# Performance work log

Hardware: AMD Instinct MI355X
Metric: run time of the kernel (lower is better)

The kernel has to match this reference:

```python
import jax, jax.numpy as jnp
import numpy as np

B, C, H, W = 16, 1024, 64, 64
CH = C // 2
LN_EPS = 1e-5  # F.layer_norm default eps

def setup_inputs() -> dict:
    key = jax.random.key(0)
    ks = jax.random.split(key, 5)
    x = jax.random.normal(ks[0], (B, C, H, W), dtype=jnp.float32)
    # 1x1 conv weights, shape (out_ch, in_ch)
    w_qr = jax.random.normal(ks[1], (1, C), dtype=jnp.float32) * 0.02
    w_vr = jax.random.normal(ks[2], (CH, C), dtype=jnp.float32) * 0.02
    w_ql = jax.random.normal(ks[3], (CH, C), dtype=jnp.float32) * 0.02
    w_vl = jax.random.normal(ks[4], (CH, C), dtype=jnp.float32) * 0.02
    return {"x": x, "w_qr": w_qr, "w_vr": w_vr, "w_ql": w_ql, "w_vl": w_vl}

def reference(x, w_qr, w_vr, w_ql, w_vl):
    b, c, h, w = x.shape
    ch, hw = c // 2, h * w
    # mmcv ConvModule: 1x1 conv (no bias, no norm) + default ReLU activation
    conv = lambda wt: jax.nn.relu(jnp.einsum('bchw,oc->bohw', x, wt))

    # --- spatial attention branch ---
    input_x = conv(w_vr).reshape(b, ch, hw)                       # (b, ch, hw)
    mask = jax.nn.softmax(conv(w_qr).reshape(b, hw), axis=1)      # (b, hw)
    context = jnp.einsum('bcn,bn->bc', input_x, mask)             # (b, ch)
    # layer_norm over (ch,1,1) -> normalize over channel dim, no affine
    mu = jnp.mean(context, axis=1, keepdims=True)
    var = jnp.mean((context - mu) ** 2, axis=1, keepdims=True)
    spatial_attn = jax.nn.sigmoid((context - mu) * jax.lax.rsqrt(var + LN_EPS))[:, :, None]  # (b, ch, 1)

    # --- channel attention branch ---
    g_x = conv(w_ql)                                              # (b, ch, h, w)
    avg_x = jax.nn.softmax(jnp.mean(g_x, axis=(2, 3)), axis=1)    # (b, ch)
    theta_x = conv(w_vl).reshape(b, ch, hw)                       # (b, ch, hw)
    channel_attn = jax.nn.sigmoid(jnp.einsum('bc,bcn->bn', avg_x, theta_x))[:, None, :]  # (b, 1, hw)

    # --- combine ---
    sequence = (spatial_attn * channel_attn).reshape(b, ch, h, w)  # outer product (b, ch, hw)
    parallel = (channel_attn + spatial_attn).reshape(b, ch, h, w)  # broadcast sum
    sk_attn = jnp.concatenate([sequence, parallel], axis=1)        # (b, c, h, w)
    return x * sk_attn + x
```

## Files before the change

### kernel.cpp

```cpp
#include <hip/hip_runtime.h>
#include <cstdint>
#include <cstddef>

#define BATCH 16
#define CIN   1024
#define CH    512
#define HW    4096

static constexpr float LN_EPS = 1e-5f;

typedef __bf16 bf16x8 __attribute__((ext_vector_type(8)));
typedef float  f32x4  __attribute__((ext_vector_type(4)));

__device__ __forceinline__ float sigmoidf_(float v) { return 1.0f / (1.0f + __expf(-v)); }

__device__ __forceinline__ unsigned short f2bf(float f) {
    union { float f; uint32_t u; } c; c.f = f;
    uint32_t r = (c.u + 0x7fffu + ((c.u >> 16) & 1u)) >> 16;
    return (unsigned short)r;
}

#define GLOAD_LDS16(g, l)                                                  \
    __builtin_amdgcn_global_load_lds(                                      \
        (const __attribute__((address_space(1))) void*)(g),                \
        (__attribute__((address_space(3))) void*)(l), 16, 0, 0)

__global__ __launch_bounds__(256) void transpose_convert(
    const float* __restrict__ x, const float* __restrict__ wqr,
    unsigned short* __restrict__ xt, float* __restrict__ maskpre)
{
    const int b  = blockIdx.z;
    const int c0 = blockIdx.y * 64;
    const int n0 = blockIdx.x * 64;
    __shared__ float t[64][65];
    const int tid = threadIdx.x;
    const int tx = tid & 15, ty = tid >> 4;
    const float* xb = x + ((size_t)b * CIN + c0) * HW + n0;
#pragma unroll
    for (int rr = 0; rr < 4; ++rr) {
        const int row = ty + rr * 16;
        float4 v = *(const float4*)(xb + (size_t)row * HW + tx * 4);
        t[row][tx * 4 + 0] = v.x; t[row][tx * 4 + 1] = v.y;
        t[row][tx * 4 + 2] = v.z; t[row][tx * 4 + 3] = v.w;
    }
    __syncthreads();
    const int n  = tid >> 2;
    const int cp = (tid & 3) * 16;
    __align__(16) unsigned short tmp[16];
    float part = 0.f;
#pragma unroll
    for (int i = 0; i < 16; ++i) {
        const float v = t[cp + i][n];
        tmp[i] = f2bf(v);
        part = fmaf(wqr[c0 + cp + i], v, part);
    }
    unsigned short* dst = xt + ((size_t)b * HW + n0 + n) * CIN + c0 + cp;
    ((uint4*)dst)[0] = ((const uint4*)tmp)[0];
    ((uint4*)dst)[1] = ((const uint4*)tmp)[1];
    part += __shfl_xor(part, 1);
    part += __shfl_xor(part, 2);
    if ((tid & 3) == 0) atomicAdd(&maskpre[(size_t)b * HW + n0 + n], part);
}

__global__ __launch_bounds__(256) void wconvert(
    const float* __restrict__ wvr, const float* __restrict__ wql,
    const float* __restrict__ wvl,
    unsigned short* __restrict__ wA, unsigned short* __restrict__ wB)
{
    const int idx = blockIdx.x * 256 + threadIdx.x;
    if (idx < 512 * 1024) {
        wA[idx] = f2bf(wql[idx]);
    } else {
        const int j = idx - 512 * 1024;
        const int row = j >> 10, col = j & 1023;
        const float v = (row < 512) ? wvr[row * 1024 + col] : wvl[(row - 512) * 1024 + col];
        wB[j] = f2bf(v);
    }
}

__global__ __launch_bounds__(512) void mfma_gemm256(
    const unsigned short* __restrict__ xt,
    const unsigned short* __restrict__ wst,
    const int MT, const int phase,
    const float* __restrict__ maskp,
    const float* __restrict__ avgx,
    float* __restrict__ gmean,
    float* __restrict__ ctx,
    float* __restrict__ cattnp)
{
    const int nwg = gridDim.x;
    const int per = nwg >> 3;
    const int bid = blockIdx.x;
    const int nid = (bid & 7) * per + (bid >> 3);
    const int mt = nid % MT;
    const int r2 = nid / MT;
    const int nb = r2 & 15;
    const int b  = r2 >> 4;
    const int o0 = mt * 256;
    const int n0 = nb * 256;

    const int tid  = threadIdx.x;
    const int w    = tid >> 6;
    const int lane = tid & 63;
    const int wm = w >> 2;
    const int wn = w & 3;
    const int lr = lane & 15;
    const int hi = lane >> 4;
    const int lr7 = lane & 7;

    __shared__ __align__(16) unsigned short lds[2 * 2 * 2 * 8192];

    f32x4 acc[8][4];
#pragma unroll
    for (int mi = 0; mi < 8; ++mi)
#pragma unroll
        for (int nj = 0; nj < 4; ++nj) acc[mi][nj] = (f32x4){0.f, 0.f, 0.f, 0.f};

    const int sr  = lane >> 3;
    const int ssl = (lane & 7) ^ sr;
    const unsigned short* gA[2][2];
    const unsigned short* gB[2][2];
#pragma unroll
    for (int h = 0; h < 2; ++h)
#pragma unroll
        for (int j = 0; j < 2; ++j) {
            const int row = (w * 2 + j) * 8 + sr;
            gA[h][j] = wst + (size_t)(o0 + h * 128 + row) * CIN + ssl * 8;
            gB[h][j] = xt + ((size_t)b * HW + n0 + h * 128 + row) * CIN + ssl * 8;
        }

#define STG(m, h, tt) do {                                                  \
        unsigned short* lb_ = lds + ((((tt) & 1) * 4) + (m) * 2 + (h)) * 8192 \
                              + (w * 2) * 512;                              \
        const unsigned short* s0_ = ((m) ? gB[h][0] : gA[h][0]) + (tt) * 64; \
        const unsigned short* s1_ = ((m) ? gB[h][1] : gA[h][1]) + (tt) * 64; \
        GLOAD_LDS16(s0_, lb_);                                              \
        GLOAD_LDS16(s1_, lb_ + 512);                                        \
    } while (0)

    const int aoff = lr * 64;
    const int boff = (wn & 1) * 4096 + lr * 64;
    const int sl0 = ((0 + hi) ^ lr7) * 8;
    const int sl1 = ((4 + hi) ^ lr7) * 8;

    bf16x8 bf[4][2];

#define PHASE_BODY(q, c, STAGE_STMT, GATE_STMT) do {                        \
        const unsigned short* Ab_ = lds + ((c) * 4 + wm) * 8192;            \
        const unsigned short* Bb_ = lds + ((c) * 4 + 2 + (wn >> 1)) * 8192; \
        if ((q) == 0) {                                                     \
            _Pragma("unroll")                                               \
            for (int nj = 0; nj < 4; ++nj) {                                \
                bf[nj][0] = *(const bf16x8*)(Bb_ + boff + nj * 1024 + sl0); \
                bf[nj][1] = *(const bf16x8*)(Bb_ + boff + nj * 1024 + sl1); \
            }                                                               \
        }                                                                   \
        bf16x8 af_[2][2];                                                   \
        _Pragma("unroll")                                                   \
        for (int mi = 0; mi < 2; ++mi) {                                    \
            af_[mi][0] = *(const bf16x8*)(Ab_ + ((q) * 32 + mi * 16) * 64 + aoff + sl0); \
            af_[mi][1] = *(const bf16x8*)(Ab_ + ((q) * 32 + mi * 16) * 64 + aoff + sl1); \
        }                                                                   \
        STAGE_STMT;                                                         \
        GATE_STMT;                                                          \
        asm volatile("s_barrier" ::: "memory");                             \
        __builtin_amdgcn_s_setprio(1);                                      \
        _Pragma("unroll")                                                   \
        for (int mi = 0; mi < 2; ++mi)                                      \
            _Pragma("unroll")                                               \
            for (int nj = 0; nj < 4; ++nj) {                                \
                acc[(q) * 2 + mi][nj] = __builtin_amdgcn_mfma_f32_16x16x32_bf16( \
                    af_[mi][0], bf[nj][0], acc[(q) * 2 + mi][nj], 0, 0, 0); \
                acc[(q) * 2 + mi][nj] = __builtin_amdgcn_mfma_f32_16x16x32_bf16( \
                    af_[mi][1], bf[nj][1], acc[(q) * 2 + mi][nj], 0, 0, 0); \
            }                                                               \
        __builtin_amdgcn_s_setprio(0);                                      \
        __builtin_amdgcn_sched_barrier(0);                                  \
        asm volatile("s_barrier" ::: "memory");                             \
    } while (0)

    STG(0, 0, 0); STG(0, 1, 0); STG(1, 0, 0); STG(1, 1, 0);
    STG(1, 0, 1); STG(1, 1, 1); STG(0, 0, 1);
    asm volatile("s_waitcnt vmcnt(6)" ::: "memory");
    asm volatile("s_barrier" ::: "memory");

#pragma unroll 2
    for (int kt = 0; kt < 16; ++kt) {
        const int c = kt & 1;
        PHASE_BODY(0, c, { if (kt < 15) STG(0, 1, kt + 1); }, {});
        PHASE_BODY(1, c, { if (kt < 14) STG(1, 0, kt + 2); }, {});
        PHASE_BODY(2, c, { if (kt < 14) STG(1, 1, kt + 2); }, {});
        PHASE_BODY(3, c, { if (kt < 14) STG(0, 0, kt + 2); },
                   { if (kt < 14)       asm volatile("s_waitcnt vmcnt(6)" ::: "memory");
                     else if (kt == 14) asm volatile("s_waitcnt vmcnt(0)" ::: "memory"); });
    }
#undef PHASE_BODY
#undef STG

    const int quad = hi;
    if (phase == 0) {
#pragma unroll
        for (int mr = 0; mr < 8; ++mr)
#pragma unroll
            for (int r = 0; r < 4; ++r) {
                float v = 0.f;
#pragma unroll
                for (int nj = 0; nj < 4; ++nj) v += fmaxf(acc[mr][nj][r], 0.f);
                v += __shfl_xor(v, 1); v += __shfl_xor(v, 2);
                v += __shfl_xor(v, 4); v += __shfl_xor(v, 8);
                if (lr == 0)
                    atomicAdd(&gmean[b * CH + o0 + wm * 128 + mr * 16 + quad * 4 + r], v);
            }
    } else if (mt < 2) {
        float mk[4];
#pragma unroll
        for (int nj = 0; nj < 4; ++nj)
            mk[nj] = maskp[(size_t)b * HW + n0 + wn * 64 + nj * 16 + lr];
#pragma unroll
        for (int mr = 0; mr < 8; ++mr)
#pragma unroll
            for (int r = 0; r < 4; ++r) {
                float v = 0.f;
#pragma unroll
                for (int nj = 0; nj < 4; ++nj)
                    v += fmaxf(acc[mr][nj][r], 0.f) * mk[nj];
                v += __shfl_xor(v, 1); v += __shfl_xor(v, 2);
                v += __shfl_xor(v, 4); v += __shfl_xor(v, 8);
                if (lr == 0)
                    atomicAdd(&ctx[b * CH + o0 + wm * 128 + mr * 16 + quad * 4 + r], v);
            }
    } else {
        float colsum[4] = {0.f, 0.f, 0.f, 0.f};
#pragma unroll
        for (int mr = 0; mr < 8; ++mr) {
            float aw[4];
#pragma unroll
            for (int r = 0; r < 4; ++r)
                aw[r] = avgx[b * CH + (o0 - 512) + wm * 128 + mr * 16 + quad * 4 + r];
#pragma unroll
            for (int nj = 0; nj < 4; ++nj)
#pragma unroll
                for (int r = 0; r < 4; ++r)
                    colsum[nj] += fmaxf(acc[mr][nj][r], 0.f) * aw[r];
        }
#pragma unroll
        for (int nj = 0; nj < 4; ++nj) {
            float v = colsum[nj];
            v += __shfl_xor(v, 16);
            v += __shfl_xor(v, 32);
            if (lane < 16)
                atomicAdd(&cattnp[(size_t)b * HW + n0 + wn * 64 + nj * 16 + lane], v);
        }
    }
}

__global__ __launch_bounds__(256) void softmax_hw_k(float* __restrict__ m)
{
    const int b = blockIdx.x;
    float* row = m + (size_t)b * HW;
    __shared__ float red[256];
    const int tid = threadIdx.x;
    float mx = 0.f;
    for (int i = tid; i < HW; i += 256) mx = fmaxf(mx, row[i]);
    red[tid] = mx; __syncthreads();
    for (int s = 128; s > 0; s >>= 1) { if (tid < s) red[tid] = fmaxf(red[tid], red[tid + s]); __syncthreads(); }
    mx = red[0]; __syncthreads();
    float sum = 0.f;
    for (int i = tid; i < HW; i += 256) { float e = __expf(fmaxf(row[i], 0.f) - mx); row[i] = e; sum += e; }
    red[tid] = sum; __syncthreads();
    for (int s = 128; s > 0; s >>= 1) { if (tid < s) red[tid] += red[tid + s]; __syncthreads(); }
    const float inv = 1.f / red[0];
    for (int i = tid; i < HW; i += 256) row[i] *= inv;
}

__global__ __launch_bounds__(256) void softmax_ch_k(const float* __restrict__ gmean,
                                                    float* __restrict__ avgx)
{
    const int b = blockIdx.x;
    const float* src = gmean + b * CH;
    float* dst = avgx + b * CH;
    __shared__ float red[256];
    const int tid = threadIdx.x;
    const float v0 = src[tid]       * (1.f / HW);
    const float v1 = src[tid + 256] * (1.f / HW);
    red[tid] = fmaxf(v0, v1); __syncthreads();
    for (int s = 128; s > 0; s >>= 1) { if (tid < s) red[tid] = fmaxf(red[tid], red[tid + s]); __syncthreads(); }
    const float mx = red[0]; __syncthreads();
    const float e0 = __expf(v0 - mx), e1 = __expf(v1 - mx);
    red[tid] = e0 + e1; __syncthreads();
    for (int s = 128; s > 0; s >>= 1) { if (tid < s) red[tid] += red[tid + s]; __syncthreads(); }
    const float inv = 1.f / red[0];
    dst[tid] = e0 * inv; dst[tid + 256] = e1 * inv;
}

__global__ __launch_bounds__(256) void ln_sig_k(const float* __restrict__ ctx,
                                                float* __restrict__ sattn)
{
    const int b = blockIdx.x;
    const float* src = ctx + b * CH;
    __shared__ float red[256];
    const int tid = threadIdx.x;
    const float v0 = src[tid], v1 = src[tid + 256];
    red[tid] = v0 + v1; __syncthreads();
    for (int s = 128; s > 0; s >>= 1) { if (tid < s) red[tid] += red[tid + s]; __syncthreads(); }
    const float mu = red[0] * (1.f / CH); __syncthreads();
    const float d0 = v0 - mu, d1 = v1 - mu;
    red[tid] = d0 * d0 + d1 * d1; __syncthreads();
    for (int s = 128; s > 0; s >>= 1) { if (tid < s) red[tid] += red[tid + s]; __syncthreads(); }
    const float rs = rsqrtf(red[0] * (1.f / CH) + LN_EPS);
    sattn[b * CH + tid]       = sigmoidf_(d0 * rs);
    sattn[b * CH + tid + 256] = sigmoidf_(d1 * rs);
}

__global__ __launch_bounds__(256) void sig_cattn_k(float* __restrict__ cattnp)
{
    const int i = blockIdx.x * 256 + threadIdx.x;
    cattnp[i] = sigmoidf_(cattnp[i]);
}

__global__ __launch_bounds__(256) void final_k(const float* __restrict__ x,
                                               const float* __restrict__ sattn,
                                               const float* __restrict__ cattnp,
                                               float* __restrict__ out)
{
    const int c = blockIdx.x;
    const int b = blockIdx.y;
    const float s = sattn[b * CH + (c & (CH - 1))];
    const bool seq = c < CH;
    const float4* xr = (const float4*)(x + ((size_t)b * CIN + c) * HW);
    const float4* cr = (const float4*)(cattnp + (size_t)b * HW);
    float4* orow = (float4*)(out + ((size_t)b * CIN + c) * HW);
    for (int i = threadIdx.x; i < HW / 4; i += 256) {
        const float4 xv = xr[i], cv = cr[i];
        float4 f;
        if (seq) { f.x = s * cv.x; f.y = s * cv.y; f.z = s * cv.z; f.w = s * cv.w; }
        else     { f.x = s + cv.x; f.y = s + cv.y; f.z = s + cv.z; f.w = s + cv.w; }
        float4 o;
        o.x = fmaf(xv.x, f.x, xv.x);
        o.y = fmaf(xv.y, f.y, xv.y);
        o.z = fmaf(xv.z, f.z, xv.z);
        o.w = fmaf(xv.w, f.w, xv.w);
        orow[i] = o;
    }
}

extern "C" void kernel_launch(void* const* d_in, const int* in_sizes, int n_in,
                              void* d_out, int out_size, void* d_ws, size_t ws_size,
                              hipStream_t stream)
{
    const float* x    = (const float*)d_in[0];
    const float* w_qr = (const float*)d_in[1];
    const float* w_vr = (const float*)d_in[2];
    const float* w_ql = (const float*)d_in[3];
    const float* w_vl = (const float*)d_in[4];
    float* out = (float*)d_out;

    unsigned short* xt = (unsigned short*)d_out;
    unsigned short* wA = xt + (size_t)BATCH * HW * CIN;
    unsigned short* wB = wA + 512 * CIN;

    float* ws     = (float*)d_ws;
    float* maskp  = ws;
    float* avgx   = maskp + BATCH * HW;
    float* sattn  = avgx  + BATCH * CH;
    float* gmean  = sattn + BATCH * CH;
    float* ctx    = gmean + BATCH * CH;
    float* cattnp = ctx   + BATCH * CH;

    hipMemsetAsync(maskp, 0,
                   (size_t)(BATCH * HW * 2 + BATCH * CH * 5) * sizeof(float), stream);

    wconvert<<<6144, 256, 0, stream>>>(w_vr, w_ql, w_vl, wA, wB);
    transpose_convert<<<dim3(HW / 64, CIN / 64, BATCH), 256, 0, stream>>>(
        x, w_qr, xt, maskp);

    mfma_gemm256<<<512, 512, 0, stream>>>(
        xt, wA, 2, 0, nullptr, nullptr, gmean, nullptr, nullptr);
    softmax_hw_k<<<BATCH, 256, 0, stream>>>(maskp);
    softmax_ch_k<<<BATCH, 256, 0, stream>>>(gmean, avgx);
    mfma_gemm256<<<1024, 512, 0, stream>>>(
        xt, wB, 4, 1, maskp, avgx, nullptr, ctx, cattnp);
    ln_sig_k<<<BATCH, 256, 0, stream>>>(ctx, sattn);
    sig_cattn_k<<<BATCH * HW / 256, 256, 0, stream>>>(cattnp);
    final_k<<<dim3(CIN, BATCH), 256, 0, stream>>>(x, sattn, cattnp, out);
}
```

Baseline: 744.9 us.

## Rebalance GEMM phases and defer spatial softmax normalization to fuse kernels

Moves the w_vr GEMM into the first GEMM launch alongside w_ql, using unnormalized exp(mask) weights so the spatial softmax denominator can be applied later in the layer-norm kernel. This removes the dependency on a full softmax pass before the context reduction. It also fuses weight conversion into the transpose kernel and merges the small softmax, layer-norm and sigmoid kernels, cutting launch count. Skipping the max subtraction in exp risks overflow for large mask logits, though the ReLU'd logits here are small.

```diff
diff --git a/kernel.cpp b/kernel.cpp
--- a/kernel.cpp
+++ b/kernel.cpp
@@ -25,15 +25,33 @@
         (const __attribute__((address_space(1))) void*)(g),                \
         (__attribute__((address_space(3))) void*)(l), 16, 0, 0)
 
-__global__ __launch_bounds__(256) void transpose_convert(
+__global__ __launch_bounds__(256) void prep_k(
     const float* __restrict__ x, const float* __restrict__ wqr,
-    unsigned short* __restrict__ xt, float* __restrict__ maskpre)
-{
-    const int b  = blockIdx.z;
-    const int c0 = blockIdx.y * 64;
-    const int n0 = blockIdx.x * 64;
+    const float* __restrict__ wvr, const float* __restrict__ wql,
+    const float* __restrict__ wvl,
+    unsigned short* __restrict__ xt, float* __restrict__ maskpre,
+    unsigned short* __restrict__ wA, unsigned short* __restrict__ wB)
+{
     __shared__ float t[64][65];
     const int tid = threadIdx.x;
+    if (blockIdx.x >= 16384) {
+        const int j = (blockIdx.x - 16384) * 256 + tid;
+        if (j < 1024 * 1024) {
+            const int row = j >> 10, col = j & 1023;
+            const float v = (row < 512) ? wql[row * 1024 + col]
+                                        : wvr[(row - 512) * 1024 + col];
+            wA[j] = f2bf(v);
+        } else {
+            const int k = j - 1024 * 1024;
+            wB[k] = f2bf(wvl[k]);
+        }
+        return;
+    }
+    const int nb = blockIdx.x & 63;
+    const int cb = (blockIdx.x >> 6) & 15;
+    const int b  = blockIdx.x >> 10;
+    const int c0 = cb * 64;
+    const int n0 = nb * 64;
     const int tx = tid & 15, ty = tid >> 4;
     const float* xb = x + ((size_t)b * CIN + c0) * HW + n0;
 #pragma unroll
@@ -60,22 +78,6 @@
     part += __shfl_xor(part, 1);
     part += __shfl_xor(part, 2);
     if ((tid & 3) == 0) atomicAdd(&maskpre[(size_t)b * HW + n0 + n], part);
-}
-
-__global__ __launch_bounds__(256) void wconvert(
-    const float* __restrict__ wvr, const float* __restrict__ wql,
-    const float* __restrict__ wvl,
-    unsigned short* __restrict__ wA, unsigned short* __restrict__ wB)
-{
-    const int idx = blockIdx.x * 256 + threadIdx.x;
-    if (idx < 512 * 1024) {
-        wA[idx] = f2bf(wql[idx]);
-    } else {
-        const int j = idx - 512 * 1024;
-        const int row = j >> 10, col = j & 1023;
-        const float v = (row < 512) ? wvr[row * 1024 + col] : wvl[(row - 512) * 1024 + col];
-        wB[j] = f2bf(v);
-    }
 }
 
 __global__ __launch_bounds__(512) void mfma_gemm256(
@@ -199,36 +201,38 @@
 
     const int quad = hi;
     if (phase == 0) {
-#pragma unroll
-        for (int mr = 0; mr < 8; ++mr)
-#pragma unroll
-            for (int r = 0; r < 4; ++r) {
-                float v = 0.f;
-#pragma unroll
-                for (int nj = 0; nj < 4; ++nj) v += fmaxf(acc[mr][nj][r], 0.f);
-                v += __shfl_xor(v, 1); v += __shfl_xor(v, 2);
-                v += __shfl_xor(v, 4); v += __shfl_xor(v, 8);
-                if (lr == 0)
-                    atomicAdd(&gmean[b * CH + o0 + wm * 128 + mr * 16 + quad * 4 + r], v);
-            }
-    } else if (mt < 2) {
-        float mk[4];
-#pragma unroll
-        for (int nj = 0; nj < 4; ++nj)
-            mk[nj] = maskp[(size_t)b * HW + n0 + wn * 64 + nj * 16 + lr];
-#pragma unroll
-        for (int mr = 0; mr < 8; ++mr)
-#pragma unroll
-            for (int r = 0; r < 4; ++r) {
-                float v = 0.f;
-#pragma unroll
-                for (int nj = 0; nj < 4; ++nj)
-                    v += fmaxf(acc[mr][nj][r], 0.f) * mk[nj];
-                v += __shfl_xor(v, 1); v += __shfl_xor(v, 2);
-                v += __shfl_xor(v, 4); v += __shfl_xor(v, 8);
-                if (lr == 0)
-                    atomicAdd(&ctx[b * CH + o0 + wm * 128 + mr * 16 + quad * 4 + r], v);
-            }
+        if (mt < 2) {
+#pragma unroll
+            for (int mr = 0; mr < 8; ++mr)
+#pragma unroll
+                for (int r = 0; r < 4; ++r) {
+                    float v = 0.f;
+#pragma unroll
+                    for (int nj = 0; nj < 4; ++nj) v += fmaxf(acc[mr][nj][r], 0.f);
+                    v += __shfl_xor(v, 1); v += __shfl_xor(v, 2);
+                    v += __shfl_xor(v, 4); v += __shfl_xor(v, 8);
+                    if (lr == 0)
+                        atomicAdd(&gmean[b * CH + o0 + wm * 128 + mr * 16 + quad * 4 + r], v);
+                }
+        } else {
+            float ew[4];
+#pragma unroll
+            for (int nj = 0; nj < 4; ++nj)
+                ew[nj] = __expf(fmaxf(maskp[(size_t)b * HW + n0 + wn * 64 + nj * 16 + lr], 0.f));
+#pragma unroll
+            for (int mr = 0; mr < 8; ++mr)
+#pragma unroll
+                for (int r = 0; r < 4; ++r) {
+                    float v = 0.f;
+#pragma unroll
+                    for (int nj = 0; nj < 4; ++nj)
+                        v += fmaxf(acc[mr][nj][r], 0.f) * ew[nj];
+                    v += __shfl_xor(v, 1); v += __shfl_xor(v, 2);
+                    v += __shfl_xor(v, 4); v += __shfl_xor(v, 8);
+                    if (lr == 0)
+                        atomicAdd(&ctx[b * CH + (o0 - 512) + wm * 128 + mr * 16 + quad * 4 + r], v);
+                }
+        }
     } else {
         float colsum[4] = {0.f, 0.f, 0.f, 0.f};
 #pragma unroll
@@ -236,7 +240,7 @@
             float aw[4];
 #pragma unroll
             for (int r = 0; r < 4; ++r)
-                aw[r] = avgx[b * CH + (o0 - 512) + wm * 128 + mr * 16 + quad * 4 + r];
+                aw[r] = avgx[b * CH + o0 + wm * 128 + mr * 16 + quad * 4 + r];
 #pragma unroll
             for (int nj = 0; nj < 4; ++nj)
 #pragma unroll
@@ -254,53 +258,54 @@
     }
 }
 
-__global__ __launch_bounds__(256) void softmax_hw_k(float* __restrict__ m)
-{
-    const int b = blockIdx.x;
-    float* row = m + (size_t)b * HW;
+__global__ __launch_bounds__(256) void smch_S_k(const float* __restrict__ gmean,
+                                                const float* __restrict__ maskp,
+                                                float* __restrict__ avgx,
+                                                float* __restrict__ sden)
+{
     __shared__ float red[256];
     const int tid = threadIdx.x;
-    float mx = 0.f;
-    for (int i = tid; i < HW; i += 256) mx = fmaxf(mx, row[i]);
-    red[tid] = mx; __syncthreads();
-    for (int s = 128; s > 0; s >>= 1) { if (tid < s) red[tid] = fmaxf(red[tid], red[tid + s]); __syncthreads(); }
-    mx = red[0]; __syncthreads();
-    float sum = 0.f;
-    for (int i = tid; i < HW; i += 256) { float e = __expf(fmaxf(row[i], 0.f) - mx); row[i] = e; sum += e; }
-    red[tid] = sum; __syncthreads();
-    for (int s = 128; s > 0; s >>= 1) { if (tid < s) red[tid] += red[tid + s]; __syncthreads(); }
-    const float inv = 1.f / red[0];
-    for (int i = tid; i < HW; i += 256) row[i] *= inv;
-}
-
-__global__ __launch_bounds__(256) void softmax_ch_k(const float* __restrict__ gmean,
-                                                    float* __restrict__ avgx)
-{
+    if (blockIdx.x < 16) {
+        const int b = blockIdx.x;
+        const float* src = gmean + b * CH;
+        float* dst = avgx + b * CH;
+        const float v0 = src[tid]       * (1.f / HW);
+        const float v1 = src[tid + 256] * (1.f / HW);
+        red[tid] = fmaxf(v0, v1); __syncthreads();
+        for (int s = 128; s > 0; s >>= 1) { if (tid < s) red[tid] = fmaxf(red[tid], red[tid + s]); __syncthreads(); }
+        const float mx = red[0]; __syncthreads();
+        const float e0 = __expf(v0 - mx), e1 = __expf(v1 - mx);
+        red[tid] = e0 + e1; __syncthreads();
+        for (int s = 128; s > 0; s >>= 1) { if (tid < s) red[tid] += red[tid + s]; __syncthreads(); }
+        const float inv = 1.f / red[0];
+        dst[tid] = e0 * inv; dst[tid + 256] = e1 * inv;
+    } else {
+        const int b = blockIdx.x - 16;
+        const float* row = maskp + (size_t)b * HW;
+        float s = 0.f;
+        for (int i = tid; i < HW; i += 256) s += __expf(fmaxf(row[i], 0.f));
+        red[tid] = s; __syncthreads();
+        for (int st = 128; st > 0; st >>= 1) { if (tid < st) red[tid] += red[tid + st]; __syncthreads(); }
+        if (tid == 0) sden[b] = red[0];
+    }
+}
+
+__global__ __launch_bounds__(256) void lnsig_k(const float* __restrict__ ctx,
+                                               const float* __restrict__ sden,
+                                               float* __restrict__ sattn,
+                                               float* __restrict__ cattnp)
+{
+    const int tid = threadIdx.x;
+    if (blockIdx.x >= 16) {
+        const int i = (blockIdx.x - 16) * 256 + tid;
+        cattnp[i] = sigmoidf_(cattnp[i]);
+        return;
+    }
     const int b = blockIdx.x;
-    const float* src = gmean + b * CH;
-    float* dst = avgx + b * CH;
-    __shared__ float red[256];
-    const int tid = threadIdx.x;
-    const float v0 = src[tid]       * (1.f / HW);
-    const float v1 = src[tid + 256] * (1.f / HW);
-    red[tid] = fmaxf(v0, v1); __syncthreads();
-    for (int s = 128; s > 0; s >>= 1) { if (tid < s) red[tid] = fmaxf(red[tid], red[tid + s]); __syncthreads(); }
-    const float mx = red[0]; __syncthreads();
-    const float e0 = __expf(v0 - mx), e1 = __expf(v1 - mx);
-    red[tid] = e0 + e1; __syncthreads();
-    for (int s = 128; s > 0; s >>= 1) { if (tid < s) red[tid] += red[tid + s]; __syncthreads(); }
-    const float inv = 1.f / red[0];
-    dst[tid] = e0 * inv; dst[tid + 256] = e1 * inv;
-}
-
-__global__ __launch_bounds__(256) void ln_sig_k(const float* __restrict__ ctx,
-                                                float* __restrict__ sattn)
-{
-    const int b = blockIdx.x;
+    const float invS = 1.f / sden[b];
     const float* src = ctx + b * CH;
     __shared__ float red[256];
-    const int tid = threadIdx.x;
-    const float v0 = src[tid], v1 = src[tid + 256];
+    const float v0 = src[tid] * invS, v1 = src[tid + 256] * invS;
     red[tid] = v0 + v1; __syncthreads();
     for (int s = 128; s > 0; s >>= 1) { if (tid < s) red[tid] += red[tid + s]; __syncthreads(); }
     const float mu = red[0] * (1.f / CH); __syncthreads();
@@ -310,12 +315,6 @@
     const float rs = rsqrtf(red[0] * (1.f / CH) + LN_EPS);
     sattn[b * CH + tid]       = sigmoidf_(d0 * rs);
     sattn[b * CH + tid + 256] = sigmoidf_(d1 * rs);
-}
-
-__global__ __launch_bounds__(256) void sig_cattn_k(float* __restrict__ cattnp)
-{
-    const int i = blockIdx.x * 256 + threadIdx.x;
-    cattnp[i] = sigmoidf_(cattnp[i]);
 }
 
 __global__ __launch_bounds__(256) void final_k(const float* __restrict__ x,
@@ -357,30 +356,27 @@
 
     unsigned short* xt = (unsigned short*)d_out;
     unsigned short* wA = xt + (size_t)BATCH * HW * CIN;
-    unsigned short* wB = wA + 512 * CIN;
+    unsigned short* wB = wA + 1024 * CIN;
 
     float* ws     = (float*)d_ws;
     float* maskp  = ws;
-    float* avgx   = maskp + BATCH * HW;
-    float* sattn  = avgx  + BATCH * CH;
-    float* gmean  = sattn + BATCH * CH;
+    float* gmean  = maskp + BATCH * HW;
     float* ctx    = gmean + BATCH * CH;
     float* cattnp = ctx   + BATCH * CH;
+    float* avgx   = cattnp + BATCH * HW;
+    float* sattn  = avgx  + BATCH * CH;
+    float* sden   = sattn + BATCH * CH;
 
     hipMemsetAsync(maskp, 0,
-                   (size_t)(BATCH * HW * 2 + BATCH * CH * 5) * sizeof(float), stream);
-
-    wconvert<<<6144, 256, 0, stream>>>(w_vr, w_ql, w_vl, wA, wB);
-    transpose_convert<<<dim3(HW / 64, CIN / 64, BATCH), 256, 0, stream>>>(
-        x, w_qr, xt, maskp);
-
+                   (size_t)(BATCH * HW * 2 + BATCH * CH * 2) * sizeof(float), stream);
+
+    prep_k<<<22528, 256, 0, stream>>>(x, w_qr, w_vr, w_ql, w_vl, xt, maskp, wA, wB);
+
+    mfma_gemm256<<<1024, 512, 0, stream>>>(
+        xt, wA, 4, 0, maskp, nullptr, gmean, ctx, nullptr);
+    smch_S_k<<<32, 256, 0, stream>>>(gmean, maskp, avgx, sden);
     mfma_gemm256<<<512, 512, 0, stream>>>(
-        xt, wA, 2, 0, nullptr, nullptr, gmean, nullptr, nullptr);
-    softmax_hw_k<<<BATCH, 256, 0, stream>>>(maskp);
-    softmax_ch_k<<<BATCH, 256, 0, stream>>>(gmean, avgx);
-    mfma_gemm256<<<1024, 512, 0, stream>>>(
-        xt, wB, 4, 1, maskp, avgx, nullptr, ctx, cattnp);
-    ln_sig_k<<<BATCH, 256, 0, stream>>>(ctx, sattn);
-    sig_cattn_k<<<BATCH * HW / 256, 256, 0, stream>>>(cattnp);
+        xt, wB, 2, 1, nullptr, avgx, nullptr, nullptr, cattnp);
+    lnsig_k<<<272, 256, 0, stream>>>(ctx, sden, sattn, cattnp);
     final_k<<<dim3(CIN, BATCH), 256, 0, stream>>>(x, sattn, cattnp, out);
 }
```

New measurement: 721.4 us. -3.2%, faster.
